# Kernel optimization log

Hardware: AMD Instinct MI355X
Metric: run time of the kernel (lower is better)

Reference implementation:

```python
import jax, jax.numpy as jnp
import numpy as np

B = 1024          # batch
S = 2048          # sparseDim == obsDim (required by PhiW shape constraints)
FISTA_ITER = 16


def setup_inputs() -> dict:
    key = jax.random.key(0)
    k1, k2, k3 = jax.random.split(key, 3)
    src = jax.random.normal(k1, (B, S, 1), dtype=jnp.float32)
    Y = jax.random.normal(k2, (B, S, 1), dtype=jnp.float32)
    W = jax.random.normal(k3, (S, S), dtype=jnp.float32)
    # F.normalize(W, p=2, dim=0): unit L2 norm per column
    W = W / jnp.linalg.norm(W, axis=0, keepdims=True)
    alpha = jnp.full((1, 1), 0.1, dtype=jnp.float32)  # alpha_initialize
    return {"src": src, "Y": Y, "W": W, "alpha": alpha}


def reference(src, Y, W, alpha):
    obsDim = W.shape[0]          # == sparseDim == S
    # Lipschitz constant: max |eig(W^T W)|; W^T W is symmetric PSD so eigvalsh is exact
    L = jnp.max(jnp.linalg.eigvalsh(W.T @ W))
    thresh = alpha / L * 0.5     # soft-threshold level, shape [1,1]

    def phiW(x):
        theta_m = x[:, :obsDim]          # [B, S, 1]
        delta = x[:, obsDim:]            # [B, S, 1]
        return src * jnp.matmul(W, theta_m) + delta

    def phiWT(y):
        return jnp.concatenate((jnp.matmul(W.T, src * y), y), axis=1)  # [B, 2S, 1]

    nb = Y.shape[0]
    x0 = jnp.zeros((nb, 2 * obsDim, 1), dtype=Y.dtype)

    def step(carry, _):
        x_old, y_k, t_old = carry
        res = Y - phiW(y_k)
        v = y_k + phiWT(res) / L
        x_new = jnp.sign(v) * jnp.maximum(jnp.abs(v) - thresh, 0.0)
        t_new = (1.0 + jnp.sqrt(1.0 + 4.0 * t_old * t_old)) / 2.0
        y_new = x_new + (t_old - 1.0) / t_new * (x_new - x_old)
        return (x_new, y_new, t_new), None

    (x_new, _, _), _ = jax.lax.scan(
        step, (x0, x0, jnp.float32(1.0)), None, length=FISTA_ITER
    )
    return x_new
```

## Files before the change

### kernel.cpp

```cpp
#include <hip/hip_runtime.h>
#include <math.h>

#define SDIM 2048
#define BATCH 1024
#define NITER 16
#define LM 40

typedef unsigned short ushort_t;
typedef __attribute__((ext_vector_type(8))) short bf16x8;
typedef __attribute__((ext_vector_type(4))) float f32x4;

#define MFMA(a,b,c) __builtin_amdgcn_mfma_f32_16x16x32_bf16((a),(b),(c),0,0,0)

__device__ __forceinline__ float softt(float v, float th){
  return copysignf(fmaxf(fabsf(v) - th, 0.0f), v);
}

__device__ __forceinline__ float bf2f(ushort_t h){
  return __uint_as_float(((unsigned)h) << 16);
}

__device__ __forceinline__ void split2(float x, ushort_t* h, ushort_t* l){
  unsigned u = __float_as_uint(x);
  unsigned hh = (u + 0x7FFFu + ((u >> 16) & 1u)) >> 16;
  float hf = __uint_as_float(hh << 16);
  float r = x - hf;
  unsigned v = __float_as_uint(r);
  unsigned ll = (v + 0x7FFFu + ((v >> 16) & 1u)) >> 16;
  *h = (ushort_t)hh; *l = (ushort_t)ll;
}

__device__ __forceinline__ void cp16(const ushort_t* g, ushort_t* l){
  __builtin_amdgcn_global_load_lds(
      (const __attribute__((address_space(1))) unsigned int*)g,
      (__attribute__((address_space(3))) unsigned int*)l, 16, 0, 0);
}

__device__ __forceinline__ void gemm_core(ushort_t* __restrict__ sm,
                                          const ushort_t* __restrict__ Ah, const ushort_t* __restrict__ Al,
                                          const ushort_t* __restrict__ Bh, const ushort_t* __restrict__ Bl,
                                          int m0, int n0, int K, f32x4 acc[2][2])
{
  constexpr int BK = 64;
  ushort_t* lAh = sm;
  ushort_t* lAl = sm + 4096;
  ushort_t* lBh = sm + 8192;
  ushort_t* lBl = sm + 12288;
  const int tid = threadIdx.x;
  const int rr = tid >> 3;
  const int kp = (tid & 7) ^ (rr & 7);
  const size_t strA = (size_t)32 * K;
  const ushort_t* gAh = Ah + (size_t)(m0 + rr) * K + kp * 8;
  const ushort_t* gAl = Al + (size_t)(m0 + rr) * K + kp * 8;
  const ushort_t* gBh = Bh + (size_t)(n0 + rr) * K + kp * 8;
  const ushort_t* gBl = Bl + (size_t)(n0 + rr) * K + kp * 8;

  const int lane = tid & 63, wv = tid >> 6;
  const int wm = (wv >> 1) * 32, wn = (wv & 1) * 32;
  const int mm = lane & 15, quad = lane >> 4;
  const int ra0 = wm + mm, ra1 = wm + 16 + mm;
  const int rb0 = wn + mm, rb1 = wn + 16 + mm;
  int oa0[2], oa1[2], ob0[2], ob1[2];
  #pragma unroll
  for (int u = 0; u < 2; u++){
    oa0[u] = ra0*BK + (((u*4 + quad) ^ (ra0 & 7)) << 3);
    oa1[u] = ra1*BK + (((u*4 + quad) ^ (ra1 & 7)) << 3);
    ob0[u] = rb0*BK + (((u*4 + quad) ^ (rb0 & 7)) << 3);
    ob1[u] = rb1*BK + (((u*4 + quad) ^ (rb1 & 7)) << 3);
  }

  const int nk = K / BK;
  cp16(gAh, &lAh[tid*8]); cp16(gAh + strA, &lAh[(tid+256)*8]);
  cp16(gAl, &lAl[tid*8]); cp16(gAl + strA, &lAl[(tid+256)*8]);
  cp16(gBh, &lBh[tid*8]); cp16(gBh + strA, &lBh[(tid+256)*8]);
  cp16(gBl, &lBl[tid*8]); cp16(gBl + strA, &lBl[(tid+256)*8]);
  gAh += BK; gAl += BK; gBh += BK; gBl += BK;

  for (int kt = 0; kt < nk; kt++){
    __syncthreads();
    bf16x8 ah0[2], ah1[2], al0[2], al1[2], bh0[2], bh1[2], bl0[2], bl1[2];
    #pragma unroll
    for (int u = 0; u < 2; u++){
      ah0[u] = *(const bf16x8*)&lAh[oa0[u]];
      ah1[u] = *(const bf16x8*)&lAh[oa1[u]];
      al0[u] = *(const bf16x8*)&lAl[oa0[u]];
      al1[u] = *(const bf16x8*)&lAl[oa1[u]];
      bh0[u] = *(const bf16x8*)&lBh[ob0[u]];
      bh1[u] = *(const bf16x8*)&lBh[ob1[u]];
      bl0[u] = *(const bf16x8*)&lBl[ob0[u]];
      bl1[u] = *(const bf16x8*)&lBl[ob1[u]];
    }
    __syncthreads();
    if (kt + 1 < nk){
      cp16(gAh, &lAh[tid*8]); cp16(gAh + strA, &lAh[(tid+256)*8]);
      cp16(gAl, &lAl[tid*8]); cp16(gAl + strA, &lAl[(tid+256)*8]);
      cp16(gBh, &lBh[tid*8]); cp16(gBh + strA, &lBh[(tid+256)*8]);
      cp16(gBl, &lBl[tid*8]); cp16(gBl + strA, &lBl[(tid+256)*8]);
      gAh += BK; gAl += BK; gBh += BK; gBl += BK;
    }
    #pragma unroll
    for (int u = 0; u < 2; u++){
      acc[0][0] = MFMA(ah0[u], bh0[u], acc[0][0]);
      acc[0][0] = MFMA(ah0[u], bl0[u], acc[0][0]);
      acc[0][0] = MFMA(al0[u], bh0[u], acc[0][0]);
      acc[0][1] = MFMA(ah0[u], bh1[u], acc[0][1]);
      acc[0][1] = MFMA(ah0[u], bl1[u], acc[0][1]);
      acc[0][1] = MFMA(al0[u], bh1[u], acc[0][1]);
      acc[1][0] = MFMA(ah1[u], bh0[u], acc[1][0]);
      acc[1][0] = MFMA(ah1[u], bl0[u], acc[1][0]);
      acc[1][0] = MFMA(al1[u], bh0[u], acc[1][0]);
      acc[1][1] = MFMA(ah1[u], bh1[u], acc[1][1]);
      acc[1][1] = MFMA(ah1[u], bl1[u], acc[1][1]);
      acc[1][1] = MFMA(al1[u], bh1[u], acc[1][1]);
    }
  }
}

__device__ __forceinline__ void gemm_coreF(ushort_t* __restrict__ sm,
    const ushort_t* __restrict__ Ah, const ushort_t* __restrict__ Al,
    const ushort_t* __restrict__ Bh, const ushort_t* __restrict__ Bl,
    int m0, int n0, int K, f32x4 acc[2][2])
{
  constexpr int BK = 64;
  const int tid = threadIdx.x;
  const int rr = tid >> 3;
  const int kp = (tid & 7) ^ (rr & 7);
  const size_t strA = (size_t)32 * K;
  const ushort_t* gAh = Ah + (size_t)(m0 + rr) * K + kp * 8;
  const ushort_t* gAl = Al + (size_t)(m0 + rr) * K + kp * 8;
  const ushort_t* gBh = Bh + (size_t)(n0 + rr) * K + kp * 8;
  const ushort_t* gBl = Bl + (size_t)(n0 + rr) * K + kp * 8;

  const int lane = tid & 63, wv = tid >> 6;
  const int wm = (wv >> 1) * 32, wn = (wv & 1) * 32;
  const int mm = lane & 15, quad = lane >> 4;
  const int ra0 = wm + mm, ra1 = wm + 16 + mm;
  const int rb0 = wn + mm, rb1 = wn + 16 + mm;
  int oa0[2], oa1[2], ob0[2], ob1[2];
  #pragma unroll
  for (int u = 0; u < 2; u++){
    oa0[u] = ra0*BK + (((u*4 + quad) ^ (ra0 & 7)) << 3);
    oa1[u] = ra1*BK + (((u*4 + quad) ^ (ra1 & 7)) << 3);
    ob0[u] = rb0*BK + (((u*4 + quad) ^ (rb0 & 7)) << 3);
    ob1[u] = rb1*BK + (((u*4 + quad) ^ (rb1 & 7)) << 3);
  }

  const int nk = K / BK;

#define STAGEF(T) { \
    ushort_t* d_ = sm + (((T) & 1) << 14); \
    const size_t o_ = (size_t)(T) * BK; \
    cp16(gAh + o_, &d_[tid*8]);          cp16(gAh + o_ + strA, &d_[(tid+256)*8]); \
    cp16(gAl + o_, &d_[4096 + tid*8]);   cp16(gAl + o_ + strA, &d_[4096 + (tid+256)*8]); \
    cp16(gBh + o_, &d_[8192 + tid*8]);   cp16(gBh + o_ + strA, &d_[8192 + (tid+256)*8]); \
    cp16(gBl + o_, &d_[12288 + tid*8]);  cp16(gBl + o_ + strA, &d_[12288 + (tid+256)*8]); \
  }

  STAGEF(0);
  for (int kt = 0; kt < nk; kt++){
    __syncthreads();
    if (kt + 1 < nk) STAGEF(kt + 1);
    const ushort_t* lAh = sm + ((kt & 1) << 14);
    const ushort_t* lAl = lAh + 4096;
    const ushort_t* lBh = lAh + 8192;
    const ushort_t* lBl = lAh + 12288;
    bf16x8 ah0[2], ah1[2], al0[2], al1[2], bh0[2], bh1[2], bl0[2], bl1[2];
    #pragma unroll
    for (int u = 0; u < 2; u++){
      ah0[u] = *(const bf16x8*)&lAh[oa0[u]];
      ah1[u] = *(const bf16x8*)&lAh[oa1[u]];
      al0[u] = *(const bf16x8*)&lAl[oa0[u]];
      al1[u] = *(const bf16x8*)&lAl[oa1[u]];
      bh0[u] = *(const bf16x8*)&lBh[ob0[u]];
      bh1[u] = *(const bf16x8*)&lBh[ob1[u]];
      bl0[u] = *(const bf16x8*)&lBl[ob0[u]];
      bl1[u] = *(const bf16x8*)&lBl[ob1[u]];
    }
    #pragma unroll
    for (int u = 0; u < 2; u++){
      acc[0][0] = MFMA(ah0[u], bh0[u], acc[0][0]);
      acc[0][0] = MFMA(ah0[u], bl0[u], acc[0][0]);
      acc[0][0] = MFMA(al0[u], bh0[u], acc[0][0]);
      acc[0][1] = MFMA(ah0[u], bh1[u], acc[0][1]);
      acc[0][1] = MFMA(ah0[u], bl1[u], acc[0][1]);
      acc[0][1] = MFMA(al0[u], bh1[u], acc[0][1]);
      acc[1][0] = MFMA(ah1[u], bh0[u], acc[1][0]);
      acc[1][0] = MFMA(ah1[u], bl0[u], acc[1][0]);
      acc[1][0] = MFMA(al1[u], bh0[u], acc[1][0]);
      acc[1][1] = MFMA(ah1[u], bh1[u], acc[1][1]);
      acc[1][1] = MFMA(ah1[u], bl1[u], acc[1][1]);
      acc[1][1] = MFMA(al1[u], bh1[u], acc[1][1]);
    }
  }
#undef STAGEF
}

__device__ __forceinline__ void acc_to_tile(ushort_t* sm, f32x4 acc[2][2]){
  float* tile = (float*)sm;
  const int tid = threadIdx.x, lane = tid & 63, wv = tid >> 6;
  const int wm = (wv >> 1) * 32, wn = (wv & 1) * 32;
  const int mm = lane & 15, quad = lane >> 4;
  #pragma unroll
  for (int tm = 0; tm < 2; tm++)
    #pragma unroll
    for (int tn = 0; tn < 2; tn++)
      #pragma unroll
      for (int i = 0; i < 4; i++)
        tile[(wm + tm*16 + quad*4 + i)*65 + wn + tn*16 + mm] = acc[tm][tn][i];
  __syncthreads();
}

#define EPILOGUE_FOR(rowvar, c4var) \
  const int tid = threadIdx.x, lane = tid & 63, wv = tid >> 6; \
  const int r4 = lane >> 4; \
  const int c4var = (lane & 15) * 4; \
  for (int j = 0; j < 4; j++){ \
    const int rowvar = wv*16 + j*4 + r4;

__global__ __launch_bounds__(256) void k_split(const float* __restrict__ W,
                                               ushort_t* __restrict__ Wah, ushort_t* __restrict__ Wal,
                                               ushort_t* __restrict__ Wbh, ushort_t* __restrict__ Wbl){
  __shared__ float t[32][33];
  const int i0 = blockIdx.y * 32, j0 = blockIdx.x * 32;
  const int r = threadIdx.x >> 3, c = (threadIdx.x & 7) * 4;
  const float4 v = *(const float4*)&W[(size_t)(i0 + r) * SDIM + j0 + c];
  float vv[4] = {v.x, v.y, v.z, v.w};
  ushort_t h[4], l[4];
  #pragma unroll
  for (int q = 0; q < 4; q++){ split2(vv[q], &h[q], &l[q]); t[r][c+q] = vv[q]; }
  *(ushort4*)&Wah[(size_t)(i0 + r) * SDIM + j0 + c] = make_ushort4(h[0],h[1],h[2],h[3]);
  *(ushort4*)&Wal[(size_t)(i0 + r) * SDIM + j0 + c] = make_ushort4(l[0],l[1],l[2],l[3]);
  __syncthreads();
  #pragma unroll
  for (int q = 0; q < 4; q++) split2(t[c+q][r], &h[q], &l[q]);
  *(ushort4*)&Wbh[(size_t)(j0 + r) * SDIM + i0 + c] = make_ushort4(h[0],h[1],h[2],h[3]);
  *(ushort4*)&Wbl[(size_t)(j0 + r) * SDIM + i0 + c] = make_ushort4(l[0],l[1],l[2],l[3]);
}

__global__ __launch_bounds__(256) void k_gemmM(const ushort_t* __restrict__ Wah, const ushort_t* __restrict__ Wal,
                                               float* __restrict__ Mmat){
  __shared__ __align__(16) ushort_t smem[16384];
  const int b = blockIdx.x + (blockIdx.y << 5);
  const int xcd = b & 7, slot = b >> 3;
  const int n0 = (((xcd << 2) + (slot & 3)) << 6);
  const int m0 = ((slot >> 2) << 6);
  f32x4 acc[2][2] = {};
  gemm_core(smem, Wah, Wal, Wah, Wal, m0, n0, SDIM, acc);
  acc_to_tile(smem, acc);
  const float* tile = (const float*)smem;
  EPILOGUE_FOR(row, c4)
    f32x4 a = *(const f32x4*)&tile[row*65 + c4];
    *(f32x4*)&Mmat[(size_t)(m0 + row) * SDIM + n0 + c4] = a;
  }
}

__global__ __launch_bounds__(256) void k_init(float* __restrict__ vRing,
                                              double* __restrict__ dotWV, double* __restrict__ dotWW,
                                              float* __restrict__ betaSq){
  __shared__ float red[256];
  int t = threadIdx.x;
  float vals[8];
  float s = 0.f;
  #pragma unroll
  for (int p = 0; p < 8; p++){
    int j = p*256 + t;
    unsigned h = (unsigned)j * 2654435761u;
    h ^= h >> 16; h *= 2246822519u; h ^= h >> 13;
    float r = (float)(h & 0xFFFFFFu) / 16777216.0f - 0.5f;
    vals[p] = r; s += r*r;
  }
  red[t] = s; __syncthreads();
  for (int o = 128; o > 0; o >>= 1){ if (t < o) red[t] += red[t+o]; __syncthreads(); }
  float inv = rsqrtf(red[0]);
  #pragma unroll
  for (int p = 0; p < 8; p++){
    int j = p*256 + t;
    vRing[SDIM + j] = vals[p]*inv;
    vRing[j] = 0.f;
    vRing[2*SDIM + j] = 0.f;
  }
  if (t < LM+2){ dotWV[t] = 0.0; dotWW[t] = 0.0; betaSq[t] = 0.f; }
}

__global__ __launch_bounds__(256) void k_lstep(const float* __restrict__ M,
    const float* __restrict__ wOld, float* __restrict__ wNew,
    float* __restrict__ vRing, double* __restrict__ dotWV, double* __restrict__ dotWW,
    float* __restrict__ betaSq, int s){
  __shared__ float vs[SDIM];
  __shared__ double pAl[4], pWw[4];
  const int tid = threadIdx.x, bid = blockIdx.x;
  if (s == 1){
    const float* v1 = vRing + SDIM;
    for (int j = tid; j < SDIM; j += 256) vs[j] = v1[j];
  } else {
    const double a  = dotWV[s-1];
    const double ww = dotWW[s-1];
    const float bpSq = betaSq[s-2];
    float bsq = (float)(ww - a*a - (double)bpSq);
    bsq = fmaxf(bsq, 1e-20f);
    const float beta = sqrtf(bsq), invb = 1.0f/beta;
    const float alpha = (float)a, bprev = sqrtf(bpSq);
    const float* vm1 = vRing + ((s-1)%3)*SDIM;
    const float* vm2 = vRing + ((s-2)%3)*SDIM;
    float* vdst = vRing + (s%3)*SDIM;
    for (int j = tid; j < SDIM; j += 256){
      float val = (wOld[j] - alpha*vm1[j] - bprev*vm2[j]) * invb;
      vs[j] = val;
      if (bid == 0) vdst[j] = val;
    }
    if (bid == 0 && tid == 0) betaSq[s-1] = bsq;
  }
  __syncthreads();
  const int wv = tid >> 6, lane = tid & 63;
  const int row = bid*4 + wv;
  const float4* Mr = (const float4*)(M + (size_t)row * SDIM);
  const float4* v4 = (const float4*)vs;
  float acc = 0.f;
  #pragma unroll
  for (int p = 0; p < 8; p++){
    int j4 = p*64 + lane;
    float4 m = Mr[j4], v = v4[j4];
    acc += m.x*v.x + m.y*v.y + m.z*v.z + m.w*v.w;
  }
  #pragma unroll
  for (int o = 32; o > 0; o >>= 1) acc += __shfl_down(acc, o);
  if (lane == 0){
    wNew[row] = acc;
    pAl[wv] = (double)acc * (double)vs[row];
    pWw[wv] = (double)acc * (double)acc;
  }
  __syncthreads();
  if (tid == 0){
    atomicAdd(&dotWV[s], pAl[0]+pAl[1]+pAl[2]+pAl[3]);
    atomicAdd(&dotWW[s], pWw[0]+pWw[1]+pWw[2]+pWw[3]);
  }
}

__global__ void k_sturm(const double* __restrict__ dotWV, const float* __restrict__ betaSq,
                        const float* __restrict__ alphaIn, float* __restrict__ Lbuf){
  __shared__ double sa[LM+1], sb[LM+1];
  int lane = threadIdx.x;
  for (int i = lane; i <= LM; i += 64){
    if (i >= 1){
      sa[i] = dotWV[i];
      sb[i] = (i < LM) ? sqrt((double)betaSq[i]) : 0.0;
    }
  }
  __syncthreads();
  double phi = -1e300, plo = 1e300;
  for (int i = 1 + lane; i <= LM; i += 64){
    double r = (i > 1 ? sb[i-1] : 0.0) + (i < LM ? sb[i] : 0.0);
    phi = fmax(phi, sa[i] + r);
    plo = fmin(plo, sa[i] - r);
  }
  for (int o = 32; o > 0; o >>= 1){
    phi = fmax(phi, __shfl_down(phi, o));
    plo = fmin(plo, __shfl_down(plo, o));
  }
  double hi = __shfl(phi, 0), lo = __shfl(plo, 0);
  for (int round = 0; round < 6; round++){
    double x = lo + (hi - lo) * (double)(lane + 1) / 65.0;
    int cnt = 0;
    double dd = sa[1] - x;
    if (dd < 0) cnt++;
    for (int i = 2; i <= LM; i++){
      double off = sb[i-1];
      if (fabs(dd) < 1e-300) dd = -1e-300;
      dd = sa[i] - x - off*off/dd;
      if (dd < 0) cnt++;
    }
    unsigned long long bal = __ballot(cnt == LM);
    int p = (bal == 0ull) ? 64 : (__ffsll((unsigned long long)bal) - 1);
    double newhi = (p <= 63) ? lo + (hi - lo) * (double)(p + 1) / 65.0 : hi;
    double newlo = (p >= 1)  ? lo + (hi - lo) * (double)p / 65.0       : lo;
    hi = newhi; lo = newlo;
  }
  if (lane == 0){
    double L = 0.5*(lo + hi);
    Lbuf[0] = (float)(1.0 / L);
    Lbuf[1] = (float)(0.5 * (double)alphaIn[0] / L);
  }
}


__global__ __launch_bounds__(256) void k_A0(const float* __restrict__ Y, const float* __restrict__ src,
                                            float* __restrict__ yd, ushort_t* __restrict__ sresh,
                                            ushort_t* __restrict__ sresl, float* __restrict__ out,
                                            const float* __restrict__ Lbuf){
  int idx = blockIdx.x*256 + threadIdx.x;
  float invL = Lbuf[0], th = Lbuf[1];
  float y = Y[idx], s = src[idx];
  split2(s*y, &sresh[idx], &sresl[idx]);
  float xn = softt(y*invL, th);
  int b = idx >> 11, i = idx & 2047;
  out[(size_t)b*4096 + 2048 + i] = xn;
  yd[idx] = xn;
}

__device__ __forceinline__ void swz512(int* m0, int* n0){
  const int b = blockIdx.x + (blockIdx.y << 5);
  const int xcd = b & 7, slot = b >> 3;
  *n0 = (((xcd << 2) + (slot & 3)) << 6);
  *m0 = ((slot >> 2) << 6);
}

__global__ __launch_bounds__(256) void k_gemmA(
    const ushort_t* __restrict__ Wah, const ushort_t* __restrict__ Wal,
    const ushort_t* __restrict__ ymh, const ushort_t* __restrict__ yml,
    const float* __restrict__ Y, const float* __restrict__ src,
    float* __restrict__ yd, float* __restrict__ out,
    ushort_t* __restrict__ sresh, ushort_t* __restrict__ sresl,
    const float* __restrict__ Lbuf, float ck)
{
  __shared__ __align__(16) ushort_t smem[32768];
  f32x4 acc[2][2] = {};
  int m0, n0; swz512(&m0, &n0);
  gemm_coreF(smem, ymh, yml, Wah, Wal, m0, n0, SDIM, acc);
  acc_to_tile(smem, acc);
  const float* tile = (const float*)smem;
  const float invL = Lbuf[0], th = Lbuf[1];
  EPILOGUE_FOR(row, c4)
    const int brow = m0 + row;
    const size_t g  = (size_t)brow*SDIM + n0 + c4;
    const size_t go = (size_t)brow*4096 + 2048 + n0 + c4;
    f32x4 a   = *(const f32x4*)&tile[row*65 + c4];
    f32x4 s4  = *(const f32x4*)&src[g];
    f32x4 y4  = *(const f32x4*)&Y[g];
    f32x4 yd4 = *(const f32x4*)&yd[g];
    f32x4 xo4 = *(const f32x4*)&out[go];
    f32x4 res, xn, yn;
    ushort4 sh, sl;
    #pragma unroll
    for (int q = 0; q < 4; q++){
      res[q] = y4[q] - s4[q]*a[q] - yd4[q];
      xn[q]  = softt(yd4[q] + res[q]*invL, th);
      yn[q]  = xn[q] + ck*(xn[q] - xo4[q]);
    }
    split2(s4[0]*res[0], &sh.x, &sl.x);
    split2(s4[1]*res[1], &sh.y, &sl.y);
    split2(s4[2]*res[2], &sh.z, &sl.z);
    split2(s4[3]*res[3], &sh.w, &sl.w);
    *(ushort4*)&sresh[g] = sh;
    *(ushort4*)&sresl[g] = sl;
    *(f32x4*)&out[go] = xn;
    *(f32x4*)&yd[g]   = yn;
  }
}

template<bool FIRST>
__global__ __launch_bounds__(256) void k_gemmB(
    const ushort_t* __restrict__ Wbh, const ushort_t* __restrict__ Wbl,
    const ushort_t* __restrict__ sresh, const ushort_t* __restrict__ sresl,
    ushort_t* __restrict__ ymh, ushort_t* __restrict__ yml,
    float* __restrict__ out, const float* __restrict__ Lbuf, float ck)
{
  __shared__ __align__(16) ushort_t smem[32768];
  f32x4 acc[2][2] = {};
  int m0, n0; swz512(&m0, &n0);
  gemm_coreF(smem, sresh, sresl, Wbh, Wbl, m0, n0, SDIM, acc);
  acc_to_tile(smem, acc);
  const float* tile = (const float*)smem;
  const float invL = Lbuf[0], th = Lbuf[1];
  EPILOGUE_FOR(row, c4)
    const int brow = m0 + row;
    const size_t g  = (size_t)brow*SDIM + n0 + c4;
    const size_t go = (size_t)brow*4096 + n0 + c4;
    f32x4 a = *(const f32x4*)&tile[row*65 + c4];
    f32x4 ym4, xo4;
    if (FIRST){
      ym4 = (f32x4){0.f,0.f,0.f,0.f};
      xo4 = (f32x4){0.f,0.f,0.f,0.f};
    } else {
      ushort4 h4 = *(const ushort4*)&ymh[g];
      ushort4 l4 = *(const ushort4*)&yml[g];
      ym4[0] = bf2f(h4.x) + bf2f(l4.x);
      ym4[1] = bf2f(h4.y) + bf2f(l4.y);
      ym4[2] = bf2f(h4.z) + bf2f(l4.z);
      ym4[3] = bf2f(h4.w) + bf2f(l4.w);
      xo4 = *(const f32x4*)&out[go];
    }
    f32x4 xn, yn;
    ushort4 hh, ll;
    #pragma unroll
    for (int q = 0; q < 4; q++){
      xn[q] = softt(ym4[q] + a[q]*invL, th);
      yn[q] = xn[q] + ck*(xn[q] - xo4[q]);
    }
    split2(yn[0], &hh.x, &ll.x);
    split2(yn[1], &hh.y, &ll.y);
    split2(yn[2], &hh.z, &ll.z);
    split2(yn[3], &hh.w, &ll.w);
    *(f32x4*)&out[go] = xn;
    *(ushort4*)&ymh[g] = hh;
    *(ushort4*)&yml[g] = ll;
  }
}


extern "C" void kernel_launch(void* const* d_in, const int* in_sizes, int n_in,
                              void* d_out, int out_size, void* d_ws, size_t ws_size,
                              hipStream_t stream) {
  const float* src   = (const float*)d_in[0];
  const float* Y     = (const float*)d_in[1];
  const float* W     = (const float*)d_in[2];
  const float* alpha = (const float*)d_in[3];
  float* out = (float*)d_out;
  float* ws  = (float*)d_ws;

  const size_t M1 = 1024*1024;
  float* Mmat = ws;
  float* yd   = ws + 4*M1;
  float* lanc = ws + 6*M1;
  float* w0      = lanc;
  float* w1      = lanc + SDIM;
  float* vRing   = lanc + 2*SDIM;
  double* dotWV  = (double*)(lanc + 5*SDIM);
  double* dotWW  = dotWV + 128;
  float* betaSq  = lanc + 5*SDIM + 512;
  float* Lbuf    = betaSq + 128;
  ushort_t* u16 = (ushort_t*)(ws + 7*M1);
  ushort_t* Wah = u16;
  ushort_t* Wal = u16 + 4*M1;
  ushort_t* Wbh = u16 + 8*M1;
  ushort_t* Wbl = u16 + 12*M1;
  ushort_t* ymh = u16 + 16*M1;
  ushort_t* yml = u16 + 18*M1;
  ushort_t* sresh = u16 + 20*M1;
  ushort_t* sresl = u16 + 22*M1;

  k_split<<<dim3(64,64), 256, 0, stream>>>(W, Wah, Wal, Wbh, Wbl);
  k_gemmM<<<dim3(32,32), 256, 0, stream>>>(Wah, Wal, Mmat);

  float* wb[2] = { w0, w1 };
  k_init<<<1, 256, 0, stream>>>(vRing, dotWV, dotWW, betaSq);
  for (int s = 1; s <= LM; s++){
    k_lstep<<<512, 256, 0, stream>>>(Mmat, wb[(s+1)&1], wb[s&1], vRing, dotWV, dotWW, betaSq, s);
  }
  k_sturm<<<1, 64, 0, stream>>>(dotWV, betaSq, alpha, Lbuf);

  double t = 1.0;
  float ckv[NITER];
  for (int k = 0; k < NITER; k++){
    double tn = 0.5*(1.0 + sqrt(1.0 + 4.0*t*t));
    ckv[k] = (float)((t - 1.0)/tn);
    t = tn;
  }

  k_A0<<<(BATCH*SDIM)/256, 256, 0, stream>>>(Y, src, yd, sresh, sresl, out, Lbuf);
  k_gemmB<true><<<dim3(32,16), 256, 0, stream>>>(Wbh, Wbl, sresh, sresl, ymh, yml, out, Lbuf, ckv[0]);
  for (int k = 1; k < NITER; k++){
    k_gemmA<<<dim3(32,16), 256, 0, stream>>>(Wah, Wal, ymh, yml, Y, src, yd, out, sresh, sresl, Lbuf, ckv[k]);
    k_gemmB<false><<<dim3(32,16), 256, 0, stream>>>(Wbh, Wbl, sresh, sresl, ymh, yml, out, Lbuf, ckv[k]);
  }
  (void)in_sizes; (void)n_in; (void)out_size; (void)ws_size;
}
```

Measured before the change: 1.680 ms.

## Fuse Lanczos iterations and Sturm bisection into one cooperative kernel

Replaces the init kernel, forty per-step Lanczos launches and the Sturm-bisection launch with a single cooperative kernel that uses grid.sync between steps, plus a memset for initialisation. The goal is to remove kernel launch overhead and inter-kernel gaps on the serial eigenvalue-estimation path. In exchange it depends on all 512 blocks being co-resident, and grid-wide barriers carry their own cost.

New measurement: 3.493 ms. +108.0%, slower.

```diff
diff --git a/kernel.cpp b/kernel.cpp
--- a/kernel.cpp
+++ b/kernel.cpp
@@ -1,4 +1,5 @@
 #include <hip/hip_runtime.h>
+#include <hip/hip_cooperative_groups.h>
 #include <math.h>
 
 #define SDIM 2048
@@ -254,131 +255,128 @@
   }
 }
 
-__global__ __launch_bounds__(256) void k_init(float* __restrict__ vRing,
-                                              double* __restrict__ dotWV, double* __restrict__ dotWW,
-                                              float* __restrict__ betaSq){
+__global__ __launch_bounds__(256) void k_lanczos(const float* __restrict__ M,
+    float* __restrict__ w0, float* __restrict__ w1,
+    float* __restrict__ vRing, double* __restrict__ dotWV, double* __restrict__ dotWW,
+    float* __restrict__ betaSq, const float* __restrict__ alphaIn, float* __restrict__ Lbuf)
+{
+  __shared__ float vs[SDIM];
   __shared__ float red[256];
-  int t = threadIdx.x;
-  float vals[8];
-  float s = 0.f;
-  #pragma unroll
-  for (int p = 0; p < 8; p++){
-    int j = p*256 + t;
-    unsigned h = (unsigned)j * 2654435761u;
-    h ^= h >> 16; h *= 2246822519u; h ^= h >> 13;
-    float r = (float)(h & 0xFFFFFFu) / 16777216.0f - 0.5f;
-    vals[p] = r; s += r*r;
-  }
-  red[t] = s; __syncthreads();
-  for (int o = 128; o > 0; o >>= 1){ if (t < o) red[t] += red[t+o]; __syncthreads(); }
-  float inv = rsqrtf(red[0]);
-  #pragma unroll
-  for (int p = 0; p < 8; p++){
-    int j = p*256 + t;
-    vRing[SDIM + j] = vals[p]*inv;
-    vRing[j] = 0.f;
-    vRing[2*SDIM + j] = 0.f;
-  }
-  if (t < LM+2){ dotWV[t] = 0.0; dotWW[t] = 0.0; betaSq[t] = 0.f; }
-}
-
-__global__ __launch_bounds__(256) void k_lstep(const float* __restrict__ M,
-    const float* __restrict__ wOld, float* __restrict__ wNew,
-    float* __restrict__ vRing, double* __restrict__ dotWV, double* __restrict__ dotWW,
-    float* __restrict__ betaSq, int s){
-  __shared__ float vs[SDIM];
   __shared__ double pAl[4], pWw[4];
+  __shared__ double sa[LM+1], sb[LM+1];
   const int tid = threadIdx.x, bid = blockIdx.x;
-  if (s == 1){
-    const float* v1 = vRing + SDIM;
-    for (int j = tid; j < SDIM; j += 256) vs[j] = v1[j];
-  } else {
-    const double a  = dotWV[s-1];
-    const double ww = dotWW[s-1];
-    const float bpSq = betaSq[s-2];
-    float bsq = (float)(ww - a*a - (double)bpSq);
-    bsq = fmaxf(bsq, 1e-20f);
-    const float beta = sqrtf(bsq), invb = 1.0f/beta;
-    const float alpha = (float)a, bprev = sqrtf(bpSq);
-    const float* vm1 = vRing + ((s-1)%3)*SDIM;
-    const float* vm2 = vRing + ((s-2)%3)*SDIM;
-    float* vdst = vRing + (s%3)*SDIM;
-    for (int j = tid; j < SDIM; j += 256){
-      float val = (wOld[j] - alpha*vm1[j] - bprev*vm2[j]) * invb;
-      vs[j] = val;
-      if (bid == 0) vdst[j] = val;
-    }
-    if (bid == 0 && tid == 0) betaSq[s-1] = bsq;
-  }
-  __syncthreads();
-  const int wv = tid >> 6, lane = tid & 63;
-  const int row = bid*4 + wv;
-  const float4* Mr = (const float4*)(M + (size_t)row * SDIM);
-  const float4* v4 = (const float4*)vs;
-  float acc = 0.f;
-  #pragma unroll
-  for (int p = 0; p < 8; p++){
-    int j4 = p*64 + lane;
-    float4 m = Mr[j4], v = v4[j4];
-    acc += m.x*v.x + m.y*v.y + m.z*v.z + m.w*v.w;
-  }
-  #pragma unroll
-  for (int o = 32; o > 0; o >>= 1) acc += __shfl_down(acc, o);
-  if (lane == 0){
-    wNew[row] = acc;
-    pAl[wv] = (double)acc * (double)vs[row];
-    pWw[wv] = (double)acc * (double)acc;
-  }
-  __syncthreads();
-  if (tid == 0){
-    atomicAdd(&dotWV[s], pAl[0]+pAl[1]+pAl[2]+pAl[3]);
-    atomicAdd(&dotWW[s], pWw[0]+pWw[1]+pWw[2]+pWw[3]);
-  }
-}
-
-__global__ void k_sturm(const double* __restrict__ dotWV, const float* __restrict__ betaSq,
-                        const float* __restrict__ alphaIn, float* __restrict__ Lbuf){
-  __shared__ double sa[LM+1], sb[LM+1];
-  int lane = threadIdx.x;
-  for (int i = lane; i <= LM; i += 64){
-    if (i >= 1){
-      sa[i] = dotWV[i];
-      sb[i] = (i < LM) ? sqrt((double)betaSq[i]) : 0.0;
-    }
-  }
-  __syncthreads();
-  double phi = -1e300, plo = 1e300;
-  for (int i = 1 + lane; i <= LM; i += 64){
-    double r = (i > 1 ? sb[i-1] : 0.0) + (i < LM ? sb[i] : 0.0);
-    phi = fmax(phi, sa[i] + r);
-    plo = fmin(plo, sa[i] - r);
-  }
-  for (int o = 32; o > 0; o >>= 1){
-    phi = fmax(phi, __shfl_down(phi, o));
-    plo = fmin(plo, __shfl_down(plo, o));
-  }
-  double hi = __shfl(phi, 0), lo = __shfl(plo, 0);
-  for (int round = 0; round < 6; round++){
-    double x = lo + (hi - lo) * (double)(lane + 1) / 65.0;
-    int cnt = 0;
-    double dd = sa[1] - x;
-    if (dd < 0) cnt++;
-    for (int i = 2; i <= LM; i++){
-      double off = sb[i-1];
-      if (fabs(dd) < 1e-300) dd = -1e-300;
-      dd = sa[i] - x - off*off/dd;
-      if (dd < 0) cnt++;
-    }
-    unsigned long long bal = __ballot(cnt == LM);
-    int p = (bal == 0ull) ? 64 : (__ffsll((unsigned long long)bal) - 1);
-    double newhi = (p <= 63) ? lo + (hi - lo) * (double)(p + 1) / 65.0 : hi;
-    double newlo = (p >= 1)  ? lo + (hi - lo) * (double)p / 65.0       : lo;
-    hi = newhi; lo = newlo;
-  }
-  if (lane == 0){
-    double L = 0.5*(lo + hi);
-    Lbuf[0] = (float)(1.0 / L);
-    Lbuf[1] = (float)(0.5 * (double)alphaIn[0] / L);
+  cooperative_groups::grid_group grid = cooperative_groups::this_grid();
+  float* wb[2] = { w0, w1 };
+
+  for (int s = 1; s <= LM; s++){
+    if (s == 1){
+      float vals[8]; float sum = 0.f;
+      #pragma unroll
+      for (int p = 0; p < 8; p++){
+        int j = p*256 + tid;
+        unsigned h = (unsigned)j * 2654435761u;
+        h ^= h >> 16; h *= 2246822519u; h ^= h >> 13;
+        float r = (float)(h & 0xFFFFFFu) / 16777216.0f - 0.5f;
+        vals[p] = r; sum += r*r;
+      }
+      red[tid] = sum; __syncthreads();
+      for (int o = 128; o > 0; o >>= 1){ if (tid < o) red[tid] += red[tid+o]; __syncthreads(); }
+      const float inv = rsqrtf(red[0]);
+      #pragma unroll
+      for (int p = 0; p < 8; p++){
+        int j = p*256 + tid;
+        vs[j] = vals[p]*inv;
+        if (bid == 0) vRing[SDIM + j] = vals[p]*inv;
+      }
+      __syncthreads();
+    } else {
+      const double a  = dotWV[s-1];
+      const double ww = dotWW[s-1];
+      const float bpSq = betaSq[s-2];
+      float bsq = (float)(ww - a*a - (double)bpSq);
+      bsq = fmaxf(bsq, 1e-20f);
+      const float beta = sqrtf(bsq), invb = 1.0f/beta;
+      const float alpha = (float)a, bprev = sqrtf(bpSq);
+      const float* wOld = wb[(s+1)&1];
+      const float* vm1 = vRing + ((s-1)%3)*SDIM;
+      const float* vm2 = vRing + ((s-2)%3)*SDIM;
+      float* vdst = vRing + (s%3)*SDIM;
+      for (int j = tid; j < SDIM; j += 256){
+        float val = (wOld[j] - alpha*vm1[j] - bprev*vm2[j]) * invb;
+        vs[j] = val;
+        if (bid == 0) vdst[j] = val;
+      }
+      if (bid == 0 && tid == 0) betaSq[s-1] = bsq;
+      __syncthreads();
+    }
+    const int wv = tid >> 6, lane = tid & 63;
+    const int row = bid*4 + wv;
+    const float4* Mr = (const float4*)(M + (size_t)row * SDIM);
+    const float4* v4 = (const float4*)vs;
+    float acc = 0.f;
+    #pragma unroll
+    for (int p = 0; p < 8; p++){
+      int j4 = p*64 + lane;
+      float4 m = Mr[j4], v = v4[j4];
+      acc += m.x*v.x + m.y*v.y + m.z*v.z + m.w*v.w;
+    }
+    #pragma unroll
+    for (int o = 32; o > 0; o >>= 1) acc += __shfl_down(acc, o);
+    if (lane == 0){
+      wb[s&1][row] = acc;
+      pAl[wv] = (double)acc * (double)vs[row];
+      pWw[wv] = (double)acc * (double)acc;
+    }
+    __syncthreads();
+    if (tid == 0){
+      atomicAdd(&dotWV[s], pAl[0]+pAl[1]+pAl[2]+pAl[3]);
+      atomicAdd(&dotWW[s], pWw[0]+pWw[1]+pWw[2]+pWw[3]);
+    }
+    grid.sync();
+  }
+
+  if (bid == 0){
+    if (tid >= 1 && tid <= LM){
+      sa[tid] = dotWV[tid];
+      sb[tid] = (tid < LM) ? sqrt((double)betaSq[tid]) : 0.0;
+    }
+    __syncthreads();
+    if (tid < 64){
+      const int lane = tid;
+      double phi = -1e300, plo = 1e300;
+      for (int i = 1 + lane; i <= LM; i += 64){
+        double r = (i > 1 ? sb[i-1] : 0.0) + (i < LM ? sb[i] : 0.0);
+        phi = fmax(phi, sa[i] + r);
+        plo = fmin(plo, sa[i] - r);
+      }
+      for (int o = 32; o > 0; o >>= 1){
+        phi = fmax(phi, __shfl_down(phi, o));
+        plo = fmin(plo, __shfl_down(plo, o));
+      }
+      double hi = __shfl(phi, 0), lo = __shfl(plo, 0);
+      for (int round = 0; round < 6; round++){
+        double x = lo + (hi - lo) * (double)(lane + 1) / 65.0;
+        int cnt = 0;
+        double dd = sa[1] - x;
+        if (dd < 0) cnt++;
+        for (int i = 2; i <= LM; i++){
+          double off = sb[i-1];
+          if (fabs(dd) < 1e-300) dd = -1e-300;
+          dd = sa[i] - x - off*off/dd;
+          if (dd < 0) cnt++;
+        }
+        unsigned long long bal = __ballot(cnt == LM);
+        int p = (bal == 0ull) ? 64 : (__ffsll((unsigned long long)bal) - 1);
+        double newhi = (p <= 63) ? lo + (hi - lo) * (double)(p + 1) / 65.0 : hi;
+        double newlo = (p >= 1)  ? lo + (hi - lo) * (double)p / 65.0       : lo;
+        hi = newhi; lo = newlo;
+      }
+      if (lane == 0){
+        double L = 0.5*(lo + hi);
+        Lbuf[0] = (float)(1.0 / L);
+        Lbuf[1] = (float)(0.5 * (double)alphaIn[0] / L);
+      }
+    }
   }
 }
 
@@ -531,12 +529,13 @@
   k_split<<<dim3(64,64), 256, 0, stream>>>(W, Wah, Wal, Wbh, Wbl);
   k_gemmM<<<dim3(32,32), 256, 0, stream>>>(Wah, Wal, Mmat);
 
-  float* wb[2] = { w0, w1 };
-  k_init<<<1, 256, 0, stream>>>(vRing, dotWV, dotWW, betaSq);
-  for (int s = 1; s <= LM; s++){
-    k_lstep<<<512, 256, 0, stream>>>(Mmat, wb[(s+1)&1], wb[s&1], vRing, dotWV, dotWW, betaSq, s);
-  }
-  k_sturm<<<1, 64, 0, stream>>>(dotWV, betaSq, alpha, Lbuf);
+  hipMemsetAsync(vRing, 0, (size_t)(3*SDIM + 640) * sizeof(float), stream);
+  {
+    void* kargs[] = { (void*)&Mmat, (void*)&w0, (void*)&w1, (void*)&vRing,
+                      (void*)&dotWV, (void*)&dotWW, (void*)&betaSq,
+                      (void*)&alpha, (void*)&Lbuf };
+    hipLaunchCooperativeKernel((void*)k_lanczos, dim3(512), dim3(256), kargs, 0, stream);
+  }
 
   double t = 1.0;
   float ckv[NITER];
```
